# Kernel tuning notes

Measured on AMD Instinct MI355X. Metric: run time of the kernel, lower is better.

## Reference

```python
import jax, jax.numpy as jnp
import numpy as np

K = 16        # neighbors (init kwarg k)
LN_EPS = 1e-5


def setup_inputs() -> dict:
    key = jax.random.key(0)
    ks = jax.random.split(key, 12)
    B, N, C, H = 4, 4096, 64, 12
    w = lambda k, s: jax.random.normal(k, s, jnp.float32) * 0.05
    d = {}
    d["x"] = jax.random.normal(ks[0], (B, N, C), jnp.float32)
    d["pos"] = jax.random.uniform(ks[1], (B, N, 3), jnp.float32)
    # to_q / to_k / to_v (bias=False). Stored as [in,out]; apply as x @ W.
    d["Wq"] = w(ks[2], (C, C)); d["Wk"] = w(ks[3], (C, C)); d["Wv"] = w(ks[4], (C, C))
    # pos_mlp: Linear(3,H) -> LayerNorm(H) -> ReLU -> Linear(H,C)
    d["p_w1"] = w(ks[5], (3, H)); d["p_b1"] = jnp.zeros((H,), jnp.float32)
    d["p_g"] = jnp.ones((H,), jnp.float32); d["p_be"] = jnp.zeros((H,), jnp.float32)
    d["p_w2"] = w(ks[6], (H, C)); d["p_b2"] = jnp.zeros((C,), jnp.float32)
    # attn_mlp: Linear(C,C) -> LayerNorm(C) -> ReLU -> Linear(C,C)
    d["a_w1"] = w(ks[7], (C, C)); d["a_b1"] = jnp.zeros((C,), jnp.float32)
    d["a_g"] = jnp.ones((C,), jnp.float32); d["a_be"] = jnp.zeros((C,), jnp.float32)
    d["a_w2"] = w(ks[8], (C, C)); d["a_b2"] = jnp.zeros((C,), jnp.float32)
    return d


def _ln(x, g, b):
    m = x.mean(-1, keepdims=True)
    v = ((x - m) ** 2).mean(-1, keepdims=True)
    return (x - m) * jax.lax.rsqrt(v + LN_EPS) * g + b


def _gather(feats, idx):
    # feats [B,N,C], idx [B,N,K] -> [B,N,K,C]
    return jax.vmap(lambda f, i: f[i])(feats, idx)


def reference(x, pos, Wq, Wk, Wv, p_w1, p_b1, p_g, p_be, p_w2, p_b2,
              a_w1, a_b1, a_g, a_be, a_w2, a_b2):
    # knn_points(pos, pos, K, return_sorted=True): K nearest by squared dist
    sq = jnp.sum(pos * pos, axis=-1)                       # [B,N]
    d2 = sq[:, :, None] + sq[:, None, :] - 2.0 * jnp.einsum('bnd,bmd->bnm', pos, pos)
    _, idx = jax.lax.top_k(-d2, K)                         # [B,N,K], ascending distance
    knn_xyz = _gather(pos, idx)                            # [B,N,K,3]
    q = x @ Wq                                             # [B,N,C]
    k = _gather(x @ Wk, idx)                               # [B,N,K,C]
    v = _gather(x @ Wv, idx)                               # [B,N,K,C]
    rel = pos[:, :, None, :] - knn_xyz                     # [B,N,K,3]
    pos_enc = jax.nn.relu(_ln(rel @ p_w1 + p_b1, p_g, p_be)) @ p_w2 + p_b2   # [B,N,K,C]
    w_in = q[:, :, None, :] - k + pos_enc                  # [B,N,K,C]
    attn = jax.nn.relu(_ln(w_in @ a_w1 + a_b1, a_g, a_be)) @ a_w2 + a_b2
    attn = jax.nn.softmax(attn, axis=-2)                   # softmax over K neighbors
    return jnp.einsum('bikd,bikd->bid', attn, v + pos_enc) # [B,N,C]
```

## Files before the change

### kernel.cpp

```cpp
#include <hip/hip_runtime.h>
#include <math.h>

#define NPTS 4096
#define KNN 16
#define LN_EPS 1e-5f

#define BOOT 128
#define CAP0 32
#define TRIG 24
#define CAP1 72
#define C1S  928
#define CHSZ 1056
#define SEG  352


__global__ __launch_bounds__(256) void proj3_kernel(
    const float* __restrict__ x, const float* __restrict__ Wq,
    const float* __restrict__ Wk, const float* __restrict__ Wv,
    float* __restrict__ qf, float* __restrict__ kf, float* __restrict__ vf) {
  int g = blockIdx.x * 256 + threadIdx.x;
  int r = g >> 6, c = g & 63;
  float sq = 0.f, sk = 0.f, sv = 0.f;
  for (int i = 0; i < 64; ++i) {
    float xv = x[r*64 + i];
    sq += xv * Wq[i*64 + c];
    sk += xv * Wk[i*64 + c];
    sv += xv * Wv[i*64 + c];
  }
  qf[g] = sq; kf[g] = sk; vf[g] = sv;
}

#define INSERT_CHAIN(DD, JJ)                                          \
  do {                                                                \
    float dd = (DD); int jj = (JJ);                                   \
    _Pragma("unroll")                                                 \
    for (int v = 0; v < 16; ++v) {                                    \
      bool sw = dd < ld[v];                                           \
      float nd = sw ? dd : ld[v]; float td = sw ? ld[v] : dd;         \
      int   nj = sw ? jj : lj[v]; int   tj = sw ? lj[v] : jj;         \
      ld[v] = nd; lj[v] = nj; dd = td; jj = tj;                       \
    }                                                                 \
  } while (0)

#define REPLAY0()                                                     \
  do {                                                                \
    float dnx = s_buf0[bo];                                           \
    float jnx = s_buf0[bo + 1];                                       \
    for (int i = 0; ; ++i) {                                          \
      unsigned long long alive = __ballot(i < cnt);                   \
      if (!alive) break;                                              \
      float dd0 = dnx; int jj0 = __float_as_int(jnx);                 \
      dnx = s_buf0[(i+1)*128 + bo];                                   \
      jnx = s_buf0[(i+1)*128 + bo + 1];                               \
      if (i < cnt && dd0 < ld[15]) INSERT_CHAIN(dd0, jj0);            \
    }                                                                 \
    cnt = 0; thr = ld[15]; s_thr[tid] = thr;                          \
  } while (0)

#define LOADP(P, SBASE)                                               \
  _Pragma("unroll")                                                   \
  for (int u = 0; u < 8; ++u) P[u] = s_p[(SBASE) + u];

#define D2V(P)                                                        \
  float d2v[8];                                                       \
  _Pragma("unroll")                                                   \
  for (int u = 0; u < 8; ++u) {                                       \
    float acc = __fmul_rn(qx, P[u].x);                                \
    acc = __fmaf_rn(qy, P[u].y, acc);                                 \
    acc = __fmaf_rn(qz, P[u].z, acc);                                 \
    d2v[u] = __fsub_rn(__fadd_rn(sqn, P[u].w), __fmul_rn(2.0f, acc)); \
  }

#define GROUP_D2(SBASE) float4 p[8]; LOADP(p, SBASE) D2V(p)

#define TREE_OFFS(THRV)                                               \
  int f0 = (d2v[0] < (THRV)) ? 1 : 0, f1 = (d2v[1] < (THRV)) ? 1 : 0, \
      f2 = (d2v[2] < (THRV)) ? 1 : 0, f3 = (d2v[3] < (THRV)) ? 1 : 0, \
      f4 = (d2v[4] < (THRV)) ? 1 : 0, f5 = (d2v[5] < (THRV)) ? 1 : 0, \
      f6 = (d2v[6] < (THRV)) ? 1 : 0, f7 = (d2v[7] < (THRV)) ? 1 : 0; \
  int s01 = f0+f1, s23 = f2+f3, s45 = f4+f5, s67 = f6+f7;             \
  int s03 = s01+s23, s47 = s45+s67;                                   \
  int o[8];                                                           \
  o[0] = cnt;        o[1] = cnt + f0;   o[2] = cnt + s01;             \
  o[3] = cnt + s01 + f2;                o[4] = cnt + s03;             \
  o[5] = o[4] + f4;  o[6] = o[4] + s45; o[7] = o[6] + f6;

#define PROC_BOOT(P, S) {                                             \
    D2V(P)                                                            \
    _Pragma("unroll")                                                 \
    for (int u = 0; u < 8; ++u) {                                     \
      float d2 = d2v[u];                                              \
      if (d2 < ld[15]) INSERT_CHAIN(d2, (S) + u);                     \
    }                                                                 \
  }

#define PROC_W0(P, S) {                                               \
    D2V(P)                                                            \
    TREE_OFFS(thr)                                                    \
    _Pragma("unroll")                                                 \
    for (int u = 0; u < 8; ++u) {                                     \
      s_buf0[o[u]*128 + bo]     = d2v[u];                             \
      s_buf0[o[u]*128 + bo + 1] = __int_as_float((S) + u);            \
    }                                                                 \
    cnt += s03 + s47;                                                 \
    int done = (S) + 8;                                               \
    bool pub = ((done & 127) == 0) && done >= 256 && done <= 896;     \
    if (pub || __ballot(cnt >= TRIG) != 0ULL) {                       \
      REPLAY0();                                                      \
      if (pub) {                                                      \
        __threadfence_block();                                        \
        s_gen = (done >> 7) - 1;                                      \
      }                                                               \
    }                                                                 \
  }

#define PROC_W13(P, S) {                                              \
    D2V(P)                                                            \
    TREE_OFFS(thrW)                                                   \
    _Pragma("unroll")                                                 \
    for (int u = 0; u < 8; ++u) {                                     \
      int oc = (o[u] <= CAP1) ? o[u] : CAP1;                          \
      jb[oc*64 + tid] = (S) + u;                                      \
    }                                                                 \
    cnt += s03 + s47;                                                 \
  }

__global__ __launch_bounds__(256) void knn_gated4_kernel(
    const float* __restrict__ pos, int* __restrict__ idx_out) {
  __shared__ __align__(16) float4 s_p[NPTS];
  __shared__ __align__(16) float  s_buf0[CAP0*128];
  __shared__ int   s_j1[3][(CAP1+1)*64];
  __shared__ float s_thr[64];
  __shared__ int   s_cnt1[3][64];
  __shared__ int   s_gen;
  __shared__ int   s_ovf;

  int t = threadIdx.x;
  int tid = t & 63, w = t >> 6, b = blockIdx.y;
  const float* pb = pos + b*NPTS*3;
  for (int j = t; j < NPTS; j += 256) {
    float px = pb[j*3+0], py = pb[j*3+1], pz = pb[j*3+2];
    float sq = __fadd_rn(__fadd_rn(__fmul_rn(px,px), __fmul_rn(py,py)),
                         __fmul_rn(pz,pz));
    s_p[j] = make_float4(px, py, pz, sq);
  }
  if (t < 64) s_thr[t] = INFINITY;
  if (t == 0) { s_ovf = 0; s_gen = 0; }
  __syncthreads();

  int n = blockIdx.x * 64 + tid;
  float4 qp = s_p[n];
  float qx = qp.x, qy = qp.y, qz = qp.z, sqn = qp.w;
  float ld[16]; int lj[16];
#pragma unroll
  for (int u = 0; u < 16; ++u) { ld[u] = INFINITY; lj[u] = 0x7fffffff; }

  float4 pA[8], pB[8];

  LOADP(pA, 0)
  for (int s = 0; s < BOOT; s += 16) {
    LOADP(pB, s + 8)
    PROC_BOOT(pA, s)
    LOADP(pA, s + 16)
    PROC_BOOT(pB, s + 8)
  }
  float thr = ld[15];
  int bo = tid << 1;
  int cnt = 0;

  if (w == 0) {
    for (int s = BOOT; s < C1S; s += 16) {
      LOADP(pB, s + 8)
      PROC_W0(pA, s)
      LOADP(pA, s + 16)
      PROC_W0(pB, s + 8)
    }
    REPLAY0();
    __syncthreads();

    int ovf = s_ovf;
    for (int ch = 0; ch < 3; ++ch) {
      int cs = C1S + ch*CHSZ;
      if (ovf & (1 << ch)) {
        int ce = cs + CHSZ;
        for (int s = cs; s < ce; s += 8) {
          GROUP_D2(s)
          TREE_OFFS(thr)
#pragma unroll
          for (int u = 0; u < 8; ++u) {
            s_buf0[o[u]*128 + bo]     = d2v[u];
            s_buf0[o[u]*128 + bo + 1] = __int_as_float(s + u);
          }
          cnt += s03 + s47;
          if (__ballot(cnt >= TRIG) != 0ULL) REPLAY0();
        }
        REPLAY0();
      } else {
        const int* jb = &s_j1[ch][0];
        int cc = s_cnt1[ch][tid];
        int jn = (0 < cc) ? jb[tid] : 0;
        float4 pn = s_p[jn];
        for (int i = 0; ; ++i) {
          unsigned long long alive = __ballot(i < cc);
          if (!alive) break;
          int jj0 = jn; float4 pj = pn;
          int ix = i + 1;
          jn = (ix < cc) ? jb[ix*64 + tid] : 0;
          pn = s_p[jn];
          if (i < cc) {
            float acc = __fmul_rn(qx, pj.x);
            acc = __fmaf_rn(qy, pj.y, acc);
            acc = __fmaf_rn(qz, pj.z, acc);
            float dd0 = __fsub_rn(__fadd_rn(sqn, pj.w), __fmul_rn(2.0f, acc));
            if (dd0 < ld[15]) INSERT_CHAIN(dd0, jj0);
          }
        }
      }
    }
    int* outp = idx_out + (b*NPTS + n)*KNN;
#pragma unroll
    for (int u = 0; u < 16; ++u) outp[u] = b*NPTS + lj[u];
  } else {
    int cs = C1S + (w-1)*CHSZ;
    int* jb = &s_j1[w-1][0];
    float thrW = thr;
#pragma unroll 1
    for (int seg = 0; seg < 3; ++seg) {
      int need = 2*seg + 2;
      while (*((volatile int*)&s_gen) < need) __builtin_amdgcn_s_sleep(2);
      thrW = fminf(thrW, *((volatile float*)&s_thr[tid]));
      int ss = cs + seg*SEG, se = ss + SEG;
      LOADP(pA, ss)
      for (int s = ss; s < se; s += 16) {
        LOADP(pB, s + 8)
        PROC_W13(pA, s)
        int sn = s + 16; if (sn >= se) sn = ss;
        LOADP(pA, sn)
        PROC_W13(pB, s + 8)
      }
    }
    s_cnt1[w-1][tid] = (cnt <= CAP1) ? cnt : CAP1;
    if (cnt > CAP1) atomicOr(&s_ovf, 1 << (w-1));
    __syncthreads();
  }
}

__device__ __forceinline__ float wsum64(float v) {
  v += __shfl_xor(v, 1);
  v += __shfl_xor(v, 2);
  v += __shfl_xor(v, 4);
  v += __shfl_xor(v, 8);
  v += __shfl_xor(v, 16);
  v += __shfl_xor(v, 32);
  return v;
}

__device__ __forceinline__ float bcast(float v, int lane) {
  return __int_as_float(__builtin_amdgcn_readlane(__float_as_int(v), lane));
}

__global__ __launch_bounds__(256) void fuse_kernel(
    const float* __restrict__ pos, const int* __restrict__ idx,
    const float* __restrict__ qf, const float* __restrict__ kf,
    const float* __restrict__ vf,
    const float* __restrict__ p_w1, const float* __restrict__ p_b1,
    const float* __restrict__ p_g, const float* __restrict__ p_be,
    const float* __restrict__ p_w2, const float* __restrict__ p_b2,
    const float* __restrict__ a_w1, const float* __restrict__ a_b1,
    const float* __restrict__ a_g, const float* __restrict__ a_be,
    const float* __restrict__ a_w2, const float* __restrict__ a_b2,
    float* __restrict__ out) {
  __shared__ __align__(16) float s_ve[16][64];
  __shared__ __align__(16) float s_t2[16][64];
  __shared__ __align__(16) float s_w1[4096];
  __shared__ __align__(16) float s_w2[4096];
  float* s_pw2 = &s_t2[0][0];
  float* s_hF  = s_pw2 + 768;
  int*   s_j   = (int*)(s_hF + 192);

  int tid = threadIdx.x;
  int p = blockIdx.x;
  int c = tid & 63, kq = tid >> 6;

  {
    const float4* w1v = (const float4*)a_w1;
    const float4* w2v = (const float4*)a_w2;
    float4* s1v = (float4*)s_w1;
    float4* s2v = (float4*)s_w2;
    for (int e = tid; e < 1024; e += 256) { s1v[e] = w1v[e]; s2v[e] = w2v[e]; }
    const float4* pwv = (const float4*)p_w2;
    float4* spv = (float4*)s_pw2;
    if (tid < 192) spv[tid] = pwv[tid];
  }

  if (tid < 16) {
    int j = idx[p*KNN + tid];
    s_j[tid] = j;
    float rx = pos[p*3+0] - pos[j*3+0];
    float ry = pos[p*3+1] - pos[j*3+1];
    float rz = pos[p*3+2] - pos[j*3+2];
    float hv[12];
    float mean = 0.f;
#pragma unroll
    for (int h = 0; h < 12; ++h) {
      float v = rx*p_w1[h] + ry*p_w1[12+h] + rz*p_w1[24+h] + p_b1[h];
      hv[h] = v; mean += v;
    }
    mean *= (1.0f/12.0f);
    float var = 0.f;
#pragma unroll
    for (int h = 0; h < 12; ++h) { float d = hv[h] - mean; var += d*d; }
    var *= (1.0f/12.0f);
    float rs = rsqrtf(var + LN_EPS);
#pragma unroll
    for (int h = 0; h < 12; ++h) {
      float a = (hv[h] - mean)*rs*p_g[h] + p_be[h];
      s_hF[tid*12 + h] = fmaxf(a, 0.f);
    }
  }
  __syncthreads();

  float win0, win1, win2, win3;
  {
    float qv = qf[p*64 + c];
    float pb2 = p_b2[c];
    float pe0 = pb2, pe1 = pb2, pe2 = pb2, pe3 = pb2;
#pragma unroll
    for (int h = 0; h < 12; ++h) {
      float wv = s_pw2[h*64 + c];
      pe0 = __fmaf_rn(s_hF[kq*12 + h],      wv, pe0);
      pe1 = __fmaf_rn(s_hF[(4+kq)*12 + h],  wv, pe1);
      pe2 = __fmaf_rn(s_hF[(8+kq)*12 + h],  wv, pe2);
      pe3 = __fmaf_rn(s_hF[(12+kq)*12 + h], wv, pe3);
    }
    int j0 = s_j[kq], j1 = s_j[4+kq], j2 = s_j[8+kq], j3 = s_j[12+kq];
    win0 = qv - kf[j0*64 + c] + pe0;  s_ve[kq][c]    = vf[j0*64 + c] + pe0;
    win1 = qv - kf[j1*64 + c] + pe1;  s_ve[4+kq][c]  = vf[j1*64 + c] + pe1;
    win2 = qv - kf[j2*64 + c] + pe2;  s_ve[8+kq][c]  = vf[j2*64 + c] + pe2;
    win3 = qv - kf[j3*64 + c] + pe3;  s_ve[12+kq][c] = vf[j3*64 + c] + pe3;
  }
  __syncthreads();

  float ab1 = a_b1[c];
  float a0 = ab1, a1 = ab1, a2 = ab1, a3 = ab1;
#pragma unroll
  for (int i = 0; i < 64; ++i) {
    float wv = s_w1[i*64 + c];
    float b0 = bcast(win0, i), b1 = bcast(win1, i);
    float b2 = bcast(win2, i), b3 = bcast(win3, i);
    a0 = __fmaf_rn(b0, wv, a0);
    a1 = __fmaf_rn(b1, wv, a1);
    a2 = __fmaf_rn(b2, wv, a2);
    a3 = __fmaf_rn(b3, wv, a3);
  }

  float ag = a_g[c], abe = a_be[c];
  float r0, r1, r2, r3;
  {
    float m = wsum64(a0) * (1.0f/64.0f); float d = a0 - m;
    float var = wsum64(d*d) * (1.0f/64.0f);
    r0 = fmaxf(d*rsqrtf(var + LN_EPS)*ag + abe, 0.f);
  }
  {
    float m = wsum64(a1) * (1.0f/64.0f); float d = a1 - m;
    float var = wsum64(d*d) * (1.0f/64.0f);
    r1 = fmaxf(d*rsqrtf(var + LN_EPS)*ag + abe, 0.f);
  }
  {
    float m = wsum64(a2) * (1.0f/64.0f); float d = a2 - m;
    float var = wsum64(d*d) * (1.0f/64.0f);
    r2 = fmaxf(d*rsqrtf(var + LN_EPS)*ag + abe, 0.f);
  }
  {
    float m = wsum64(a3) * (1.0f/64.0f); float d = a3 - m;
    float var = wsum64(d*d) * (1.0f/64.0f);
    r3 = fmaxf(d*rsqrtf(var + LN_EPS)*ag + abe, 0.f);
  }

  float ab2 = a_b2[c];
  float t0 = ab2, t1 = ab2, t2 = ab2, t3 = ab2;
#pragma unroll
  for (int i = 0; i < 64; ++i) {
    float wv = s_w2[i*64 + c];
    float b0 = bcast(r0, i), b1 = bcast(r1, i);
    float b2 = bcast(r2, i), b3 = bcast(r3, i);
    t0 = __fmaf_rn(b0, wv, t0);
    t1 = __fmaf_rn(b1, wv, t1);
    t2 = __fmaf_rn(b2, wv, t2);
    t3 = __fmaf_rn(b3, wv, t3);
  }
  s_t2[kq][c]    = t0;
  s_t2[4+kq][c]  = t1;
  s_t2[8+kq][c]  = t2;
  s_t2[12+kq][c] = t3;
  __syncthreads();

  if (tid < 64) {
    float mx = -INFINITY;
    for (int k = 0; k < 16; ++k) mx = fmaxf(mx, s_t2[k][tid]);
    float se = 0.f, po = 0.f;
    for (int k = 0; k < 16; ++k) {
      float e = expf(s_t2[k][tid] - mx);
      se += e; po += e * s_ve[k][tid];
    }
    out[p*64 + tid] = po / se;
  }
}

extern "C" void kernel_launch(void* const* d_in, const int* in_sizes, int n_in,
                              void* d_out, int out_size, void* d_ws, size_t ws_size,
                              hipStream_t stream) {
  const float* x    = (const float*)d_in[0];
  const float* pos  = (const float*)d_in[1];
  const float* Wq   = (const float*)d_in[2];
  const float* Wk   = (const float*)d_in[3];
  const float* Wv   = (const float*)d_in[4];
  const float* p_w1 = (const float*)d_in[5];
  const float* p_b1 = (const float*)d_in[6];
  const float* p_g  = (const float*)d_in[7];
  const float* p_be = (const float*)d_in[8];
  const float* p_w2 = (const float*)d_in[9];
  const float* p_b2 = (const float*)d_in[10];
  const float* a_w1 = (const float*)d_in[11];
  const float* a_b1 = (const float*)d_in[12];
  const float* a_g  = (const float*)d_in[13];
  const float* a_be = (const float*)d_in[14];
  const float* a_w2 = (const float*)d_in[15];
  const float* a_b2 = (const float*)d_in[16];

  float* ws   = (float*)d_ws;
  float* qf   = ws;
  float* kf   = qf + 1048576;
  float* vf   = kf + 1048576;
  int*   idx  = (int*)(vf + 1048576);
  float* outp = (float*)d_out;

  hipLaunchKernelGGL(proj3_kernel, dim3(4096), dim3(256), 0, stream,
                     x, Wq, Wk, Wv, qf, kf, vf);
  hipLaunchKernelGGL(knn_gated4_kernel, dim3(64, 4), dim3(256), 0, stream,
                     pos, idx);
  hipLaunchKernelGGL(fuse_kernel, dim3(16384), dim3(256), 0, stream,
                     pos, idx, qf, kf, vf,
                     p_w1, p_b1, p_g, p_be, p_w2, p_b2,
                     a_w1, a_b1, a_g, a_be, a_w2, a_b2, outp);
}
```

Baseline: 431.0 us.

## Share one LDS weight buffer and parallelize softmax across all waves

The fuse kernel now reuses a single 16KB LDS buffer for a_w1 and then a_w2, roughly halving shared memory per block so more blocks can be resident per CU. The a_w2 load is issued after the first matmul, with extra barriers added around it. The value+pos_enc terms stay in registers, and the softmax over K is split across all four waves with partial max/sum/product reductions, instead of one wave looping over 16 neighbors. The cost is two extra barriers and exposed a_w2 load latency within each block.

```diff
diff --git a/kernel.cpp b/kernel.cpp
--- a/kernel.cpp
+++ b/kernel.cpp
@@ -270,13 +270,14 @@
     const float* __restrict__ a_g, const float* __restrict__ a_be,
     const float* __restrict__ a_w2, const float* __restrict__ a_b2,
     float* __restrict__ out) {
-  __shared__ __align__(16) float s_ve[16][64];
-  __shared__ __align__(16) float s_t2[16][64];
-  __shared__ __align__(16) float s_w1[4096];
-  __shared__ __align__(16) float s_w2[4096];
-  float* s_pw2 = &s_t2[0][0];
-  float* s_hF  = s_pw2 + 768;
-  int*   s_j   = (int*)(s_hF + 192);
+  __shared__ __align__(16) float s_w[4096];
+  __shared__ __align__(16) float s_x[1024];
+  float* s_pw2 = s_x;
+  float* s_hF  = s_x + 768;
+  int*   s_j   = (int*)(s_x + 960);
+  float (*s_rm)[64] = (float(*)[64])(s_x);
+  float (*s_rs)[64] = (float(*)[64])(s_x + 256);
+  float (*s_rp)[64] = (float(*)[64])(s_x + 512);
 
   int tid = threadIdx.x;
   int p = blockIdx.x;
@@ -284,10 +285,8 @@
 
   {
     const float4* w1v = (const float4*)a_w1;
-    const float4* w2v = (const float4*)a_w2;
-    float4* s1v = (float4*)s_w1;
-    float4* s2v = (float4*)s_w2;
-    for (int e = tid; e < 1024; e += 256) { s1v[e] = w1v[e]; s2v[e] = w2v[e]; }
+    float4* sv = (float4*)s_w;
+    for (int e = tid; e < 1024; e += 256) sv[e] = w1v[e];
     const float4* pwv = (const float4*)p_w2;
     float4* spv = (float4*)s_pw2;
     if (tid < 192) spv[tid] = pwv[tid];
@@ -321,6 +320,7 @@
   __syncthreads();
 
   float win0, win1, win2, win3;
+  float ve0, ve1, ve2, ve3;
   {
     float qv = qf[p*64 + c];
     float pb2 = p_b2[c];
@@ -334,10 +334,10 @@
       pe3 = __fmaf_rn(s_hF[(12+kq)*12 + h], wv, pe3);
     }
     int j0 = s_j[kq], j1 = s_j[4+kq], j2 = s_j[8+kq], j3 = s_j[12+kq];
-    win0 = qv - kf[j0*64 + c] + pe0;  s_ve[kq][c]    = vf[j0*64 + c] + pe0;
-    win1 = qv - kf[j1*64 + c] + pe1;  s_ve[4+kq][c]  = vf[j1*64 + c] + pe1;
-    win2 = qv - kf[j2*64 + c] + pe2;  s_ve[8+kq][c]  = vf[j2*64 + c] + pe2;
-    win3 = qv - kf[j3*64 + c] + pe3;  s_ve[12+kq][c] = vf[j3*64 + c] + pe3;
+    win0 = qv - kf[j0*64 + c] + pe0;  ve0 = vf[j0*64 + c] + pe0;
+    win1 = qv - kf[j1*64 + c] + pe1;  ve1 = vf[j1*64 + c] + pe1;
+    win2 = qv - kf[j2*64 + c] + pe2;  ve2 = vf[j2*64 + c] + pe2;
+    win3 = qv - kf[j3*64 + c] + pe3;  ve3 = vf[j3*64 + c] + pe3;
   }
   __syncthreads();
 
@@ -345,7 +345,7 @@
   float a0 = ab1, a1 = ab1, a2 = ab1, a3 = ab1;
 #pragma unroll
   for (int i = 0; i < 64; ++i) {
-    float wv = s_w1[i*64 + c];
+    float wv = s_w[i*64 + c];
     float b0 = bcast(win0, i), b1 = bcast(win1, i);
     float b2 = bcast(win2, i), b3 = bcast(win3, i);
     a0 = __fmaf_rn(b0, wv, a0);
@@ -353,6 +353,13 @@
     a2 = __fmaf_rn(b2, wv, a2);
     a3 = __fmaf_rn(b3, wv, a3);
   }
+  __syncthreads();
+
+  {
+    const float4* w2v = (const float4*)a_w2;
+    float4* sv = (float4*)s_w;
+    for (int e = tid; e < 1024; e += 256) sv[e] = w2v[e];
+  }
 
   float ag = a_g[c], abe = a_be[c];
   float r0, r1, r2, r3;
@@ -376,12 +383,13 @@
     float var = wsum64(d*d) * (1.0f/64.0f);
     r3 = fmaxf(d*rsqrtf(var + LN_EPS)*ag + abe, 0.f);
   }
+  __syncthreads();
 
   float ab2 = a_b2[c];
   float t0 = ab2, t1 = ab2, t2 = ab2, t3 = ab2;
 #pragma unroll
   for (int i = 0; i < 64; ++i) {
-    float wv = s_w2[i*64 + c];
+    float wv = s_w[i*64 + c];
     float b0 = bcast(r0, i), b1 = bcast(r1, i);
     float b2 = bcast(r2, i), b3 = bcast(r3, i);
     t0 = __fmaf_rn(b0, wv, t0);
@@ -389,20 +397,20 @@
     t2 = __fmaf_rn(b2, wv, t2);
     t3 = __fmaf_rn(b3, wv, t3);
   }
-  s_t2[kq][c]    = t0;
-  s_t2[4+kq][c]  = t1;
-  s_t2[8+kq][c]  = t2;
-  s_t2[12+kq][c] = t3;
-  __syncthreads();
-
+
+  s_rm[kq][c] = fmaxf(fmaxf(t0, t1), fmaxf(t2, t3));
+  __syncthreads();
+  float mx = fmaxf(fmaxf(s_rm[0][c], s_rm[1][c]),
+                   fmaxf(s_rm[2][c], s_rm[3][c]));
+  float e0 = expf(t0 - mx), e1 = expf(t1 - mx);
+  float e2 = expf(t2 - mx), e3 = expf(t3 - mx);
+  s_rs[kq][c] = ((e0 + e1) + e2) + e3;
+  s_rp[kq][c] = __fmaf_rn(e3, ve3, __fmaf_rn(e2, ve2,
+                __fmaf_rn(e1, ve1, e0*ve0)));
+  __syncthreads();
   if (tid < 64) {
-    float mx = -INFINITY;
-    for (int k = 0; k < 16; ++k) mx = fmaxf(mx, s_t2[k][tid]);
-    float se = 0.f, po = 0.f;
-    for (int k = 0; k < 16; ++k) {
-      float e = expf(s_t2[k][tid] - mx);
-      se += e; po += e * s_ve[k][tid];
-    }
+    float se = ((s_rs[0][tid] + s_rs[1][tid]) + s_rs[2][tid]) + s_rs[3][tid];
+    float po = ((s_rp[0][tid] + s_rp[1][tid]) + s_rp[2][tid]) + s_rp[3][tid];
     out[p*64 + tid] = po / se;
   }
 }
```

New measurement: 443.0 us. +2.8%, slower.
